# Kernel tuning notes

Measured on AMD Instinct MI355X. Metric: run time of the kernel, lower is better.

## Reference

```python
import jax, jax.numpy as jnp
import numpy as np

BIT = 64
N_CLASS = 100
NUM_TRAIN = 100000
BATCH = 512
MU = 1.0   # config['mu']
M = 1.0    # config['m']
ETA = 0.5  # config['eta']
VUL = 1.0  # config['vul']
NTA = 1.0  # config['nta']


def setup_inputs() -> dict:
    key = jax.random.key(0)
    k1, k2, k3, k4, k5, k6 = jax.random.split(key, 6)
    u = jax.random.normal(k1, (BATCH, BIT), jnp.float32)
    # y / Y are one-hot label matrices in DFH; build realistic one-hot floats
    labels = jax.random.randint(k2, (BATCH,), 0, N_CLASS)
    y = jax.nn.one_hot(labels, N_CLASS, dtype=jnp.float32)
    ind = jax.random.randint(k3, (BATCH,), 0, NUM_TRAIN)
    U = jax.random.normal(k4, (BIT, NUM_TRAIN), jnp.float32)
    train_labels = jax.random.randint(k5, (NUM_TRAIN,), 0, N_CLASS)
    Y = jax.nn.one_hot(train_labels, N_CLASS, dtype=jnp.float32).T  # [n_class, num_train]
    V = jax.random.normal(k6, (BIT, N_CLASS), jnp.float32)
    return {"u": u, "y": y, "ind": ind, "U": U, "Y": Y, "V": V}


def _center_gradient(V, y, b):
    # 200-step gradient descent on V minimizing intra + vul*inter + nta*quant.
    n_class = V.shape[1]
    TK = V.shape[0] * (2.0 * jnp.eye(n_class, dtype=V.dtype)
                       - jnp.ones((n_class, n_class), V.dtype))
    yt = y.T  # [n_class, batch]

    def inner_loss(Vc):
        intra = jnp.mean((Vc @ yt - b) ** 2)
        inter = jnp.mean((Vc.T @ Vc - TK) ** 2)
        quant = jnp.mean((Vc - jnp.sign(Vc)) ** 2)
        return intra + VUL * inter + NTA * quant

    grad_fn = jax.grad(inner_loss)

    def step(Vc, i):
        # torch code multiplies alpha by 0.1 *before* the update at i==149 and i==179
        alpha = 0.03 * jnp.where(i >= 149, 0.1, 1.0) * jnp.where(i >= 179, 0.1, 1.0)
        return Vc - alpha * grad_fn(Vc), None

    V_new, _ = jax.lax.scan(step, V, jnp.arange(200))
    return V_new


def reference(u, y, ind, U, Y, V):
    # state buffer updates (torch: self.U[:, ind] = u.t().data, etc.)
    U = U.at[:, ind].set(u.T)
    Y = Y.at[:, ind].set(y.T)
    C = jnp.sign(V)
    b = jnp.sign(MU * (C @ y.T) + u.T)                     # [bit, batch]
    V_new = _center_gradient(V, y, b)                      # updated self.V
    s = (y @ Y > 0).astype(u.dtype)                        # [batch, num_train]
    ip = jnp.clip(0.5 * (u @ U), -100.0, 50.0)             # [batch, num_train]
    metric_loss = jnp.mean((1.0 - s) * jnp.log1p(jnp.exp(M + ip))
                           + s * jnp.log1p(jnp.exp(M - ip)))
    quantization_loss = jnp.mean((b - u.T) ** 2)
    loss = metric_loss + ETA * quantization_loss
    return loss, V_new
```

## Files before the change

kernel.cpp:

```cpp
#include <hip/hip_runtime.h>

#define BIT 64
#define NCLASS 100
#define NTRAIN 100000
#define BATCH 512

#define O_OWNER   0
#define O_LAB     200000
#define O_UT      200512
#define O_BSUM    233280
#define O_COUNT   239680
#define O_QSUM    239780
#define O_MSUM    239782

typedef __attribute__((ext_vector_type(8))) short short8v;
typedef __attribute__((ext_vector_type(4))) float f32x4;
typedef unsigned short ushortT;

__device__ __forceinline__ float signf(float x) {
    return (x > 0.f) ? 1.f : ((x < 0.f) ? -1.f : 0.f);
}

__device__ __forceinline__ unsigned cvtpk(float lo, float hi) {
    unsigned r;
    asm("v_cvt_pk_bf16_f32 %0, %1, %2" : "=v"(r) : "v"(lo), "v"(hi));
    return r;
}
__device__ __forceinline__ float dpp_x1(float x) {
    union { float f; int i; } v; v.f = x;
    v.i = __builtin_amdgcn_mov_dpp(v.i, 0xB1, 0xF, 0xF, false);
    return v.f;
}
__device__ __forceinline__ float dpp_x2(float x) {
    union { float f; int i; } v; v.f = x;
    v.i = __builtin_amdgcn_mov_dpp(v.i, 0x4E, 0xF, 0xF, false);
    return v.f;
}

__global__ __launch_bounds__(512) void k_pre(
        const float* __restrict__ y, const int* __restrict__ ind,
        const float* __restrict__ u, const float* __restrict__ V,
        int* owner, int* lab, float* Bsum, float* count, double* qsum,
        float* uT) {
    __shared__ float srow[BATCH];
    __shared__ int   labl[BATCH];
    __shared__ double wq[8];
    const int r = blockIdx.x;
    const int bb = threadIdx.x;

    const float* yrow = y + bb * NCLASS;
    int best = 0;
    for (int c = 0; c < NCLASS; ++c)
        if (yrow[c] > 0.5f) best = c;
    labl[bb] = best;
    if (r == 0) {
        lab[bb] = best;
        atomicMax(&owner[ind[bb]], bb);
    }

    const float v  = V[r * NCLASS + best];
    const float uu = u[bb * BIT + r];
    uT[r * BATCH + bb] = uu;
    const float bv = signf(signf(v) + uu);
    srow[bb] = bv;
    const float d = bv - uu;
    double q = (double)(d * d);
    for (int off = 32; off; off >>= 1) q += __shfl_down(q, off);
    const int wid = bb >> 6, lane = bb & 63;
    if (lane == 0) wq[wid] = q;
    __syncthreads();
    if (bb == 0) {
        double s = 0;
        for (int w = 0; w < 8; ++w) s += wq[w];
        atomicAdd(qsum, s);
    }

    if (bb < NCLASS) {
        float s = 0.f; int n = 0;
        for (int k = 0; k < BATCH; ++k) {
            const bool hit = (labl[k] == bb);
            s += hit ? srow[k] : 0.f;
            n += hit;
        }
        Bsum[r * NCLASS + bb] = s;
        if (r == 0) count[bb] = (float)n;
    }
}

__global__ __launch_bounds__(512, 2) void k_main(
        const float* __restrict__ V, const float* __restrict__ Bsum,
        const float* __restrict__ count, const float* __restrict__ u,
        const float* __restrict__ U, const float* __restrict__ Y,
        const int* __restrict__ lab, const int* __restrict__ owner,
        const float* __restrict__ uT, double* msum, float* __restrict__ out) {
    __shared__ __align__(16) char smem[70144];

    if (blockIdx.x == 0) {
        ushortT* SAb = (ushortT*)smem;
        ushortT* SBb = (ushortT*)(smem + 32768);
        ushortT* SMf = (ushortT*)(smem + 61440);
        float*   rs  = (float*)(smem + 69632);

        const int t = threadIdx.x, l = t & 63, w = t >> 6;
        const int g = l >> 4, c16 = l & 15;
        const int h = w >> 2;
        const int mtile = w & 3;
        const int m = mtile * 16 + c16;
        const bool dg = ((mtile >> 1) == h);
        const short8v ONES = {0x3F80,0x3F80,0x3F80,0x3F80,
                              0x3F80,0x3F80,0x3F80,0x3F80};

        for (int i = t; i < 16384; i += 512) SAb[i] = 0;
        for (int i = t; i < 14336; i += 512) SBb[i] = 0;

        const float ci = 2.0f / 32768.0f;
        const float ce = 4.0f / 10000.0f;
        const float cq = 2.0f / 6400.0f;
        const float ce64 = 64.0f * ce;

        bool live[4], wact[4];
        int sbO[4];
        float vreg[4][4], Kc[4][4], ncib[4][4];
        #pragma unroll
        for (int q = 0; q < 4; ++q) {
            const int nt = 4 * h + q;
            const int n0 = nt * 16 + 4 * g;
            wact[q] = (nt < 7);
            live[q] = wact[q] && (n0 < NCLASS);
            sbO[q] = ((nt * 2 + (mtile >> 1)) * 64 +
                      (16 * (c16 >> 2) + 4 * g + (c16 & 3))) * 8 + 4 * (mtile & 1);
            #pragma unroll
            for (int r = 0; r < 4; ++r) {
                float v = 0.f, bs = 0.f, cn = 0.f;
                if (live[q]) {
                    const int n = n0 + r;
                    v  = V[m * NCLASS + n];
                    bs = Bsum[m * NCLASS + n];
                    cn = count[n];
                }
                vreg[q][r] = v;
                Kc[q][r]   = ci * cn + cq - 128.f * ce;
                ncib[q][r] = -ci * bs;
            }
        }
        const int saO0 = (mtile * 4 + 2 * h) * 512 + l * 8;
        const int saO1 = saO0 + 512;

        uint4 waA, waB;

        auto store_frags = [&](ushortT* SAn, ushortT* SBn) {
            waA.x = cvtpk(vreg[0][0], vreg[0][1]);
            waA.y = cvtpk(vreg[0][2], vreg[0][3]);
            waA.z = cvtpk(vreg[1][0], vreg[1][1]);
            waA.w = cvtpk(vreg[1][2], vreg[1][3]);
            *(uint4*)&SAn[saO0] = waA;
            waB.x = cvtpk(vreg[2][0], vreg[2][1]);
            waB.y = cvtpk(vreg[2][2], vreg[2][3]);
            waB.z = cvtpk(vreg[3][0], vreg[3][1]);
            waB.w = cvtpk(vreg[3][2], vreg[3][3]);
            *(uint4*)&SAn[saO1] = waB;
            #pragma unroll
            for (int q = 0; q < 4; ++q) {
                if (wact[q]) {
                    float a0 = vreg[q][0], a1 = vreg[q][1];
                    float a2 = vreg[q][2], a3 = vreg[q][3];
                    float t0 = dpp_x1(a1), t1 = dpp_x1(a0);
                    float t2 = dpp_x1(a3), t3 = dpp_x1(a2);
                    const bool o1 = (l & 1);
                    float c0 = o1 ? t0 : a0;
                    float c1 = o1 ? a1 : t1;
                    float c2 = o1 ? t2 : a2;
                    float c3 = o1 ? a3 : t3;
                    float u0 = dpp_x2(c2), u1 = dpp_x2(c3);
                    float u2 = dpp_x2(c0), u3 = dpp_x2(c1);
                    const bool o2 = (l & 2);
                    float d0 = o2 ? u0 : c0;
                    float d1 = o2 ? u1 : c1;
                    float d2 = o2 ? c2 : u2;
                    float d3 = o2 ? c3 : u3;
                    uint2 wb;
                    wb.x = cvtpk(d0, d1);
                    wb.y = cvtpk(d2, d3);
                    *(uint2*)&SBn[sbO[q]] = wb;
                }
            }
        };

        __syncthreads();
        store_frags(SAb, SBb);
        __syncthreads();

        int cur = 0;
        for (int step = 0; step < 200; ++step) {
            float alpha = 0.03f;
            if (step >= 149) alpha *= 0.1f;
            if (step >= 179) alpha *= 0.1f;

            const ushortT* SAc = SAb + cur * 8192;

            f32x4 aM0 = {0.f,0.f,0.f,0.f}, aM1 = {0.f,0.f,0.f,0.f};
            f32x4 aR  = {0.f,0.f,0.f,0.f};
            #pragma unroll
            for (int ks = 0; ks < 4; ++ks) {
                short8v b  = *(const short8v*)&SAc[mtile * 2048 + ks * 512 + l * 8];
                short8v a0 = *(const short8v*)&SAc[(2 * h) * 2048 + ks * 512 + l * 8];
                short8v a1 = *(const short8v*)&SAc[(2 * h + 1) * 2048 + ks * 512 + l * 8];
                aM0 = __builtin_amdgcn_mfma_f32_16x16x32_bf16(a0, b, aM0, 0, 0, 0);
                aM1 = __builtin_amdgcn_mfma_f32_16x16x32_bf16(a1, b, aM1, 0, 0, 0);
                if (dg)
                    aR = __builtin_amdgcn_mfma_f32_16x16x32_bf16(b, ONES, aR, 0, 0, 0);
            }
            {
                uint4 sm;
                sm.x = cvtpk(aM0[0], aM0[1]);
                sm.y = cvtpk(aM0[2], aM0[3]);
                sm.z = cvtpk(aM1[0], aM1[1]);
                sm.w = cvtpk(aM1[2], aM1[3]);
                *(uint4*)&SMf[(mtile * 2 + h) * 512 + l * 8] = sm;
            }
            if (dg && c16 == 0)
                *(f32x4*)&rs[mtile * 16 + 4 * g] = aR;
            __syncthreads();

            const ushortT* SBc = SBb + cur * 7168;
            f32x4 p[4];
            #pragma unroll
            for (int q = 0; q < 4; ++q) p[q] = (f32x4){0.f,0.f,0.f,0.f};
            #pragma unroll
            for (int kb = 0; kb < 2; ++kb) {
                short8v bP = *(const short8v*)&SMf[(mtile * 2 + kb) * 512 + l * 8];
                #pragma unroll
                for (int q = 0; q < 4; ++q) {
                    if (wact[q]) {
                        short8v aP = *(const short8v*)
                            &SBc[((4 * h + q) * 2 + kb) * 512 + l * 8];
                        p[q] = __builtin_amdgcn_mfma_f32_16x16x32_bf16(aP, bP, p[q], 0, 0, 0);
                    }
                }
            }
            const float rsm = rs[m];

            #pragma unroll
            for (int q = 0; q < 4; ++q) {
                if (wact[q]) {
                    #pragma unroll
                    for (int r = 0; r < 4; ++r) {
                        const float v = vreg[q][r];
                        float t1 = __builtin_fmaf(Kc[q][r], v, ncib[q][r]);
                        t1 = __builtin_fmaf(ce,   p[q][r], t1);
                        t1 = __builtin_fmaf(ce64, rsm,     t1);
                        t1 -= __builtin_copysignf(cq, v);
                        float vn = __builtin_fmaf(-alpha, t1, v);
                        vreg[q][r] = live[q] ? vn : 0.f;
                    }
                }
            }
            store_frags(SAb + (cur ^ 1) * 8192, SBb + (cur ^ 1) * 7168);
            __syncthreads();
            cur ^= 1;
        }

        #pragma unroll
        for (int q = 0; q < 4; ++q) {
            if (live[q]) {
                const int n0 = (4 * h + q) * 16 + 4 * g;
                #pragma unroll
                for (int r = 0; r < 4; ++r)
                    out[1 + m * NCLASS + n0 + r] = vreg[q][r];
            }
        }
    } else {
        double* wsum = (double*)(smem);
        int*    tls  = (int*)(smem + 64);

        const int t = threadIdx.x;
        const int jj = t & 255;
        const int j = (blockIdx.x - 1) * 256 + jj;
        const int half = t >> 8;
        const bool jok = (j < NTRAIN);

        if (half == 0) {
            int tl = 0;
            if (jok) {
                for (int c = 0; c < NCLASS; ++c)
                    if (Y[(size_t)c * NTRAIN + j] > 0.5f) tl = c;
                int ow = owner[j];
                if (ow >= 0) tl = lab[ow];
            }
            tls[jj] = tl;
        }
        __syncthreads();
        const int tl = tls[jj];

        const float* colbase = U;
        size_t cstride = NTRAIN;
        if (jok) {
            int ow = owner[j];
            if (ow >= 0) { colbase = u + (size_t)ow * BIT; cstride = 1; }
            else         { colbase = U + j; }
        }

        float lsum = 0.f;
        for (int ch = 0; ch < 4; ++ch) {
            const int b0u = __builtin_amdgcn_readfirstlane((half * 4 + ch) * 64);

            if (jok) {
                float acc[64];
                #pragma unroll
                for (int k = 0; k < 64; ++k) acc[k] = 0.f;
                #pragma unroll 4
                for (int r = 0; r < BIT; ++r) {
                    float Uv = colbase[(size_t)r * cstride];
                    const float* urow = &uT[r * BATCH + b0u];
                    #pragma unroll
                    for (int qq = 0; qq < 16; ++qq) {
                        float4 uv = *(const float4*)&urow[qq * 4];
                        acc[4 * qq + 0] += uv.x * Uv;
                        acc[4 * qq + 1] += uv.y * Uv;
                        acc[4 * qq + 2] += uv.z * Uv;
                        acc[4 * qq + 3] += uv.w * Uv;
                    }
                }
                #pragma unroll
                for (int k = 0; k < 64; ++k) {
                    const int lv = lab[b0u + k];
                    float ip = fminf(fmaxf(0.5f * acc[k], -100.f), 50.f);
                    float x = (lv == tl) ? (1.0f - ip) : (1.0f + ip);
                    lsum += fmaxf(x, 0.f) + __logf(1.f + __expf(-fabsf(x)));
                }
            }
        }

        double d = (double)lsum;
        for (int off = 32; off; off >>= 1) d += __shfl_down(d, off);
        const int wid = t >> 6, lane = t & 63;
        if (lane == 0) wsum[wid] = d;
        __syncthreads();
        if (t == 0) {
            double s = 0;
            for (int ww = 0; ww < 8; ++ww) s += wsum[ww];
            atomicAdd(msum, s);
        }
    }
}

__global__ void k_final(const double* __restrict__ msum,
                        const double* __restrict__ qsum, float* out) {
    if (threadIdx.x == 0) {
        double loss = (*msum) / ((double)BATCH * (double)NTRAIN)
                    + 0.5 * ((*qsum) / ((double)BIT * (double)BATCH));
        out[0] = (float)loss;
    }
}

extern "C" void kernel_launch(void* const* d_in, const int* in_sizes, int n_in,
                              void* d_out, int out_size, void* d_ws, size_t ws_size,
                              hipStream_t stream) {
    const float* u   = (const float*)d_in[0];
    const float* y   = (const float*)d_in[1];
    const int*   ind = (const int*)d_in[2];
    const float* U   = (const float*)d_in[3];
    const float* Y   = (const float*)d_in[4];
    const float* V   = (const float*)d_in[5];
    float* out = (float*)d_out;

    int*   wsI = (int*)d_ws;
    float* wsF = (float*)d_ws;
    int*   owner = wsI + O_OWNER;
    int*   lab   = wsI + O_LAB;
    float* uT    = wsF + O_UT;
    float* Bsum  = wsF + O_BSUM;
    float* count = wsF + O_COUNT;
    double* qsum = (double*)(wsF + O_QSUM);
    double* msum = (double*)(wsF + O_MSUM);

    hipMemsetAsync(owner, 0xFF, NTRAIN * sizeof(int), stream);
    hipMemsetAsync(wsF + O_QSUM, 0, 4 * sizeof(float), stream);

    k_pre<<<64, 512, 0, stream>>>(y, ind, u, V, owner, lab, Bsum, count, qsum, uT);
    k_main<<<1 + (NTRAIN + 255) / 256, 512, 0, stream>>>(
        V, Bsum, count, u, U, Y, lab, owner, uT, msum, out);
    k_final<<<1, 64, 0, stream>>>(msum, qsum, out);
}
```

Before: 436.3 us.

## Stage transposed u tiles in LDS per chunk instead of global uT buffer

The metric blocks now transpose each 64-row chunk of u into padded shared memory (stride 68) every chunk, rather than reading a global uT buffer written by k_pre. Labels are also cached in shared memory, and launch bounds are raised to 4 blocks per SM with a trimmed register set (wact array dropped). The aim is to turn repeated global/L2 float4 loads into LDS reads and to raise occupancy. The cost is extra syncthreads and a per-block staging pass of 8192 elements per chunk, plus possible register spills from the tighter launch bound with a 64-float accumulator array.

```diff
diff --git a/kernel.cpp b/kernel.cpp
--- a/kernel.cpp
+++ b/kernel.cpp
@@ -7,7 +7,6 @@
 
 #define O_OWNER   0
 #define O_LAB     200000
-#define O_UT      200512
 #define O_BSUM    233280
 #define O_COUNT   239680
 #define O_QSUM    239780
@@ -40,8 +39,7 @@
 __global__ __launch_bounds__(512) void k_pre(
         const float* __restrict__ y, const int* __restrict__ ind,
         const float* __restrict__ u, const float* __restrict__ V,
-        int* owner, int* lab, float* Bsum, float* count, double* qsum,
-        float* uT) {
+        int* owner, int* lab, float* Bsum, float* count, double* qsum) {
     __shared__ float srow[BATCH];
     __shared__ int   labl[BATCH];
     __shared__ double wq[8];
@@ -60,7 +58,6 @@
 
     const float v  = V[r * NCLASS + best];
     const float uu = u[bb * BIT + r];
-    uT[r * BATCH + bb] = uu;
     const float bv = signf(signf(v) + uu);
     srow[bb] = bv;
     const float d = bv - uu;
@@ -87,13 +84,13 @@
     }
 }
 
-__global__ __launch_bounds__(512, 2) void k_main(
+__global__ __launch_bounds__(512, 4) void k_main(
         const float* __restrict__ V, const float* __restrict__ Bsum,
         const float* __restrict__ count, const float* __restrict__ u,
         const float* __restrict__ U, const float* __restrict__ Y,
         const int* __restrict__ lab, const int* __restrict__ owner,
-        const float* __restrict__ uT, double* msum, float* __restrict__ out) {
-    __shared__ __align__(16) char smem[70144];
+        double* msum, float* __restrict__ out) {
+    __shared__ __align__(16) char smem[69888];
 
     if (blockIdx.x == 0) {
         ushortT* SAb = (ushortT*)smem;
@@ -118,15 +115,15 @@
         const float cq = 2.0f / 6400.0f;
         const float ce64 = 64.0f * ce;
 
-        bool live[4], wact[4];
+        bool live[4];
         int sbO[4];
         float vreg[4][4], Kc[4][4], ncib[4][4];
         #pragma unroll
         for (int q = 0; q < 4; ++q) {
             const int nt = 4 * h + q;
             const int n0 = nt * 16 + 4 * g;
-            wact[q] = (nt < 7);
-            live[q] = wact[q] && (n0 < NCLASS);
+            const bool wact = (nt < 7);
+            live[q] = wact && (n0 < NCLASS);
             sbO[q] = ((nt * 2 + (mtile >> 1)) * 64 +
                       (16 * (c16 >> 2) + 4 * g + (c16 & 3))) * 8 + 4 * (mtile & 1);
             #pragma unroll
@@ -146,22 +143,21 @@
         const int saO0 = (mtile * 4 + 2 * h) * 512 + l * 8;
         const int saO1 = saO0 + 512;
 
-        uint4 waA, waB;
-
         auto store_frags = [&](ushortT* SAn, ushortT* SBn) {
-            waA.x = cvtpk(vreg[0][0], vreg[0][1]);
-            waA.y = cvtpk(vreg[0][2], vreg[0][3]);
-            waA.z = cvtpk(vreg[1][0], vreg[1][1]);
-            waA.w = cvtpk(vreg[1][2], vreg[1][3]);
-            *(uint4*)&SAn[saO0] = waA;
-            waB.x = cvtpk(vreg[2][0], vreg[2][1]);
-            waB.y = cvtpk(vreg[2][2], vreg[2][3]);
-            waB.z = cvtpk(vreg[3][0], vreg[3][1]);
-            waB.w = cvtpk(vreg[3][2], vreg[3][3]);
-            *(uint4*)&SAn[saO1] = waB;
+            uint4 wa;
+            wa.x = cvtpk(vreg[0][0], vreg[0][1]);
+            wa.y = cvtpk(vreg[0][2], vreg[0][3]);
+            wa.z = cvtpk(vreg[1][0], vreg[1][1]);
+            wa.w = cvtpk(vreg[1][2], vreg[1][3]);
+            *(uint4*)&SAn[saO0] = wa;
+            wa.x = cvtpk(vreg[2][0], vreg[2][1]);
+            wa.y = cvtpk(vreg[2][2], vreg[2][3]);
+            wa.z = cvtpk(vreg[3][0], vreg[3][1]);
+            wa.w = cvtpk(vreg[3][2], vreg[3][3]);
+            *(uint4*)&SAn[saO1] = wa;
             #pragma unroll
             for (int q = 0; q < 4; ++q) {
-                if (wact[q]) {
+                if (4 * h + q < 7) {
                     float a0 = vreg[q][0], a1 = vreg[q][1];
                     float a2 = vreg[q][2], a3 = vreg[q][3];
                     float t0 = dpp_x1(a1), t1 = dpp_x1(a0);
@@ -231,7 +227,7 @@
                 short8v bP = *(const short8v*)&SMf[(mtile * 2 + kb) * 512 + l * 8];
                 #pragma unroll
                 for (int q = 0; q < 4; ++q) {
-                    if (wact[q]) {
+                    if (4 * h + q < 7) {
                         short8v aP = *(const short8v*)
                             &SBc[((4 * h + q) * 2 + kb) * 512 + l * 8];
                         p[q] = __builtin_amdgcn_mfma_f32_16x16x32_bf16(aP, bP, p[q], 0, 0, 0);
@@ -242,7 +238,7 @@
 
             #pragma unroll
             for (int q = 0; q < 4; ++q) {
-                if (wact[q]) {
+                if (4 * h + q < 7) {
                     #pragma unroll
                     for (int r = 0; r < 4; ++r) {
                         const float v = vreg[q][r];
@@ -270,14 +266,17 @@
             }
         }
     } else {
-        double* wsum = (double*)(smem);
-        int*    tls  = (int*)(smem + 64);
+        float*  ut   = (float*)smem;
+        int*    slab = (int*)(smem + 34816);
+        double* wsum = (double*)(smem + 36864);
+        int*    tls  = (int*)(smem + 36928);
 
         const int t = threadIdx.x;
         const int jj = t & 255;
         const int j = (blockIdx.x - 1) * 256 + jj;
         const int half = t >> 8;
         const bool jok = (j < NTRAIN);
+        slab[t] = lab[t];
 
         if (half == 0) {
             int tl = 0;
@@ -302,16 +301,22 @@
 
         float lsum = 0.f;
         for (int ch = 0; ch < 4; ++ch) {
-            const int b0u = __builtin_amdgcn_readfirstlane((half * 4 + ch) * 64);
+            __syncthreads();
+            for (int i = t; i < 8192; i += 512) {
+                int buf = i >> 12, k = (i >> 6) & 63, r = i & 63;
+                ut[buf * 4352 + r * 68 + k] = u[((buf * 4 + ch) * 64 + k) * BIT + r];
+            }
+            __syncthreads();
 
             if (jok) {
+                const float* myut = ut + half * 4352;
                 float acc[64];
                 #pragma unroll
                 for (int k = 0; k < 64; ++k) acc[k] = 0.f;
-                #pragma unroll 4
+                #pragma unroll 2
                 for (int r = 0; r < BIT; ++r) {
                     float Uv = colbase[(size_t)r * cstride];
-                    const float* urow = &uT[r * BATCH + b0u];
+                    const float* urow = &myut[r * 68];
                     #pragma unroll
                     for (int qq = 0; qq < 16; ++qq) {
                         float4 uv = *(const float4*)&urow[qq * 4];
@@ -321,11 +326,11 @@
                         acc[4 * qq + 3] += uv.w * Uv;
                     }
                 }
+                const int b0 = (half * 4 + ch) * 64;
                 #pragma unroll
                 for (int k = 0; k < 64; ++k) {
-                    const int lv = lab[b0u + k];
                     float ip = fminf(fmaxf(0.5f * acc[k], -100.f), 50.f);
-                    float x = (lv == tl) ? (1.0f - ip) : (1.0f + ip);
+                    float x = (slab[b0 + k] == tl) ? (1.0f - ip) : (1.0f + ip);
                     lsum += fmaxf(x, 0.f) + __logf(1.f + __expf(-fabsf(x)));
                 }
             }
@@ -368,7 +373,6 @@
     float* wsF = (float*)d_ws;
     int*   owner = wsI + O_OWNER;
     int*   lab   = wsI + O_LAB;
-    float* uT    = wsF + O_UT;
     float* Bsum  = wsF + O_BSUM;
     float* count = wsF + O_COUNT;
     double* qsum = (double*)(wsF + O_QSUM);
@@ -377,8 +381,8 @@
     hipMemsetAsync(owner, 0xFF, NTRAIN * sizeof(int), stream);
     hipMemsetAsync(wsF + O_QSUM, 0, 4 * sizeof(float), stream);
 
-    k_pre<<<64, 512, 0, stream>>>(y, ind, u, V, owner, lab, Bsum, count, qsum, uT);
+    k_pre<<<64, 512, 0, stream>>>(y, ind, u, V, owner, lab, Bsum, count, qsum);
     k_main<<<1 + (NTRAIN + 255) / 256, 512, 0, stream>>>(
-        V, Bsum, count, u, U, Y, lab, owner, uT, msum, out);
+        V, Bsum, count, u, U, Y, lab, owner, msum, out);
     k_final<<<1, 64, 0, stream>>>(msum, qsum, out);
 }
```

Measured after the change: 364.6 us (median of 2 runs). 16.4% less time.
